# Kernel tuning notes

Measured on AMD Instinct MI355X. Metric: run time of the kernel, lower is better.

The kernel has to match this reference:

```python
import jax, jax.numpy as jnp
import numpy as np

N, E, F_IN, H, C, L = 50000, 800000, 128, 128, 47, 3
BN_EPS = 1e-5


def setup_inputs() -> dict:
    key = jax.random.key(0)
    ks = jax.random.split(key, 12)
    s = 0.1
    return {
        "x": jax.random.normal(ks[0], (N, F_IN), jnp.float32),
        "edge_index": jax.random.randint(ks[1], (2, E), 0, N, jnp.int32),
        # stacked GINConv MLP params (in_channels == hidden so all layers stack)
        "W1": jax.random.normal(ks[2], (L, F_IN, H), jnp.float32) * s,
        "b1": jnp.full((L, H), 0.01, jnp.float32),
        "gamma": jnp.ones((L, H), jnp.float32),
        "beta": jnp.zeros((L, H), jnp.float32),
        "bn_mean": jnp.zeros((L, H), jnp.float32),
        "bn_var": jnp.ones((L, H), jnp.float32),
        "W2": jax.random.normal(ks[3], (L, H, H), jnp.float32) * s,
        "b2": jnp.full((L, H), 0.01, jnp.float32),
        # head
        "lw1": jax.random.normal(ks[4], (H, H), jnp.float32) * s,
        "lb1": jnp.zeros((H,), jnp.float32),
        "lw2": jax.random.normal(ks[5], (H, C), jnp.float32) * s,
        "lb2": jnp.zeros((C,), jnp.float32),
    }


def reference(x, edge_index, W1, b1, gamma, beta, bn_mean, bn_var, W2, b2, lw1, lb1, lw2, lb2):
    src, dst = edge_index[0], edge_index[1]
    h = x
    for i in range(L):
        # GINConv: nn((1 + eps) * x + sum_{j in N(i)} x_j), eps = 0
        agg = jax.ops.segment_sum(h[src], dst, num_segments=N)  # [N, H] scatter-sum
        z = agg + h
        z = z @ W1[i] + b1[i]
        # BatchNorm1d in eval mode (running stats)
        z = (z - bn_mean[i]) * jax.lax.rsqrt(bn_var[i] + BN_EPS) * gamma[i] + beta[i]
        z = jax.nn.relu(z)
        h = jax.nn.relu(z @ W2[i] + b2[i])
    h = jax.nn.relu(h @ lw1 + lb1)
    # dropout disabled (eval mode)
    logits = h @ lw2 + lb2
    return jax.nn.log_softmax(logits, axis=-1)
```

## Files before the change

### kernel.cpp

```cpp
#include <hip/hip_runtime.h>
#include <math.h>

#define NN 50000
#define EE 800000
#define HH 128
#define LL 3
#define CC 47
#define CAP 64
#define FILL_B 2048
#define NT_TILES 782

typedef _Float16 half8 __attribute__((ext_vector_type(8)));
typedef float    f32x4 __attribute__((ext_vector_type(4)));
typedef float    f32x2 __attribute__((ext_vector_type(2)));
typedef unsigned int   u32x2 __attribute__((ext_vector_type(2)));
typedef unsigned short us8 __attribute__((ext_vector_type(8)));

__device__ __forceinline__ f32x4 mfma16(half8 a, half8 b, f32x4 c) {
    return __builtin_amdgcn_mfma_f32_16x16x32_f16(a, b, c, 0, 0, 0);
}

__device__ __forceinline__ void acc8_from_fp8(u32x2 w, float* a) {
    f32x2 p0 = __builtin_amdgcn_cvt_pk_f32_fp8(w[0], false);
    f32x2 p1 = __builtin_amdgcn_cvt_pk_f32_fp8(w[0], true);
    f32x2 p2 = __builtin_amdgcn_cvt_pk_f32_fp8(w[1], false);
    f32x2 p3 = __builtin_amdgcn_cvt_pk_f32_fp8(w[1], true);
    a[0] += p0[0]; a[1] += p0[1]; a[2] += p1[0]; a[3] += p1[1];
    a[4] += p2[0]; a[5] += p2[1]; a[6] += p3[0]; a[7] += p3[1];
}
__device__ __forceinline__ u32x2 pack8_fp8(const float* z) {
    unsigned int lo = __builtin_amdgcn_cvt_pk_fp8_f32(z[0], z[1], 0, false);
    lo = (unsigned int)__builtin_amdgcn_cvt_pk_fp8_f32(z[2], z[3], (int)lo, true);
    unsigned int hi = __builtin_amdgcn_cvt_pk_fp8_f32(z[4], z[5], 0, false);
    hi = (unsigned int)__builtin_amdgcn_cvt_pk_fp8_f32(z[6], z[7], (int)hi, true);
    u32x2 w; w[0] = lo; w[1] = hi;
    return w;
}

__global__ void k_fill_prep(const int* __restrict__ ei, int* __restrict__ cursor,
                            unsigned short* __restrict__ csr,
                            const float* __restrict__ x, const float* __restrict__ W1,
                            const float* __restrict__ W2, const float* __restrict__ lw1,
                            const float* __restrict__ lw2, const float* __restrict__ b1,
                            const float* __restrict__ gamma, const float* __restrict__ beta,
                            const float* __restrict__ bnm, const float* __restrict__ bnv,
                            unsigned char* __restrict__ x8, unsigned char* __restrict__ h8a,
                            unsigned char* __restrict__ h8b, _Float16* __restrict__ Wt1h,
                            _Float16* __restrict__ Wt2h, _Float16* __restrict__ lw1t,
                            _Float16* __restrict__ lw2t, float* __restrict__ A1f,
                            float* __restrict__ B1f) {
    if (blockIdx.x < FILL_B) {
        const int part = blockIdx.x & 7;
        const int chunk = blockIdx.x >> 3;
        const int nchunks = FILL_B >> 3;
        const int lo = part * (NN / 8);
        const int hi = (part == 7) ? NN : lo + (NN / 8);
        for (int e = chunk * 256 + threadIdx.x; e < EE; e += nchunks * 256) {
            const int d = ei[EE + e];
            if (d >= lo && d < hi) {
                const int pos = atomicAdd(&cursor[d], 1);
                if (pos < CAP) csr[(d << 6) + pos] = (unsigned short)ei[e];
            }
        }
        return;
    }
    const int i = (blockIdx.x - FILL_B) * 256 + threadIdx.x;
    const int Q0 = (NN * HH) / 8;
    const int Q1 = Q0 + LL * HH * HH;
    const int Q2 = Q1 + LL * HH * HH;
    const int Q3 = Q2 + HH * HH;
    const int Q4 = Q3 + 48 * HH;
    const int Q5 = Q4 + LL * HH;
    const int Q6 = Q5 + 3 * HH;
    if (i < Q0) {
        const f32x4* xp = (const f32x4*)x + (size_t)i * 2;
        f32x4 u = xp[0], v = xp[1];
        float z[8] = {u[0], u[1], u[2], u[3], v[0], v[1], v[2], v[3]};
        ((u32x2*)x8)[i] = pack8_fp8(z);
    } else if (i < Q1) {
        int j = i - Q0;
        int l = j / (HH * HH);
        int n = (j / HH) % HH;
        int k = j % HH;
        Wt1h[l * HH * HH + n * HH + k] = (_Float16)W1[l * HH * HH + k * HH + n];
    } else if (i < Q2) {
        int j = i - Q1;
        int l = j / (HH * HH);
        int n = (j / HH) % HH;
        int k = j % HH;
        Wt2h[l * HH * HH + n * HH + k] = (_Float16)W2[l * HH * HH + k * HH + n];
    } else if (i < Q3) {
        int j = i - Q2;
        int n = j / HH, k = j % HH;
        lw1t[n * HH + k] = (_Float16)lw1[k * HH + n];
    } else if (i < Q4) {
        int j = i - Q3;
        int n = j / HH, k = j % HH;
        lw2t[n * HH + k] = (_Float16)((n < CC) ? lw2[k * CC + n] : 0.f);
    } else if (i < Q5) {
        int j = i - Q4;
        float s = gamma[j] * rsqrtf(bnv[j] + 1e-5f);
        A1f[j] = s;
        B1f[j] = (b1[j] - bnm[j]) * s + beta[j];
    } else if (i < Q6) {
        int j = i - Q5;
        int b = j >> 7, k = j & 127;
        unsigned char* t = (b == 0) ? x8 : ((b == 1) ? h8a : h8b);
        t[(size_t)NN * HH + k] = 0;
    }
}

__device__ __forceinline__ void gather_tile8(
    const unsigned char* __restrict__ hin8, const int* __restrict__ degs,
    const unsigned short* __restrict__ csr, _Float16* Ab, int tile0, int tid, int fo) {
#pragma unroll
    for (int pass = 0; pass < 4; ++pass) {
        const int r = pass * 16 + (tid >> 4);
        const int g = tile0 + r;
        const int gg = (g < NN) ? g : NN;
        float a[8] = {0.f, 0.f, 0.f, 0.f, 0.f, 0.f, 0.f, 0.f};
        u32x2 hv = *(const u32x2*)(hin8 + (size_t)gg * HH + fo);
        acc8_from_fp8(hv, a);
        int d = (g < NN) ? degs[g] : 0;
        d = (d < CAP) ? d : CAP;
        const unsigned short* crow = csr + (gg << 6);
        for (int kk = 0; kk < d; kk += 8) {
            us8 sv = *(const us8*)(crow + kk);
            int s[8];
#pragma unroll
            for (int j = 0; j < 8; ++j) s[j] = (kk + j < d) ? (int)sv[j] : NN;
            u32x2 v[8];
#pragma unroll
            for (int j = 0; j < 8; ++j) v[j] = *(const u32x2*)(hin8 + (size_t)s[j] * HH + fo);
#pragma unroll
            for (int j = 0; j < 8; ++j) acc8_from_fp8(v[j], a);
        }
        half8 o;
#pragma unroll
        for (int j = 0; j < 8; ++j) o[j] = (_Float16)a[j];
        *(half8*)(Ab + r * 136 + fo) = o;
    }
}

__global__ __launch_bounds__(256, 4) void k_layer(
    const unsigned char* __restrict__ hin8, unsigned char* __restrict__ hout8,
    const _Float16* __restrict__ Wt1, const _Float16* __restrict__ Wt2,
    const float* __restrict__ A1, const float* __restrict__ B1,
    const float* __restrict__ b2, const int* __restrict__ degs,
    const unsigned short* __restrict__ csr) {
    __shared__ _Float16 Ab[64 * 136];
    const int tid = threadIdx.x;
    const int wave = tid >> 6, lane = tid & 63;
    const int q = lane >> 4, l15 = lane & 15;
    const int tile0 = blockIdx.x * 64;
    const int fo = (tid & 15) * 8;

    half8 Bf[2][4];
#pragma unroll
    for (int t = 0; t < 2; ++t)
#pragma unroll
        for (int kt = 0; kt < 4; ++kt)
            Bf[t][kt] = *(const half8*)(Wt1 + (wave * 32 + t * 16 + l15) * 128 + kt * 32 + q * 8);

    gather_tile8(hin8, degs, csr, Ab, tile0, tid, fo);
    __syncthreads();

    f32x4 acc[4][2];
#pragma unroll
    for (int s = 0; s < 4; ++s)
#pragma unroll
        for (int t = 0; t < 2; ++t) acc[s][t] = (f32x4){0.f, 0.f, 0.f, 0.f};
#pragma unroll
    for (int kt = 0; kt < 4; ++kt) {
        const int ko = kt * 32 + q * 8;
        half8 a0 = *(const half8*)(Ab + (0 * 16 + l15) * 136 + ko);
        half8 a1 = *(const half8*)(Ab + (1 * 16 + l15) * 136 + ko);
        half8 a2 = *(const half8*)(Ab + (2 * 16 + l15) * 136 + ko);
        half8 a3 = *(const half8*)(Ab + (3 * 16 + l15) * 136 + ko);
        acc[0][0] = mfma16(a0, Bf[0][kt], acc[0][0]);
        acc[1][0] = mfma16(a1, Bf[0][kt], acc[1][0]);
        acc[2][0] = mfma16(a2, Bf[0][kt], acc[2][0]);
        acc[3][0] = mfma16(a3, Bf[0][kt], acc[3][0]);
        acc[0][1] = mfma16(a0, Bf[1][kt], acc[0][1]);
        acc[1][1] = mfma16(a1, Bf[1][kt], acc[1][1]);
        acc[2][1] = mfma16(a2, Bf[1][kt], acc[2][1]);
        acc[3][1] = mfma16(a3, Bf[1][kt], acc[3][1]);
    }
#pragma unroll
    for (int t = 0; t < 2; ++t)
#pragma unroll
        for (int kt = 0; kt < 4; ++kt)
            Bf[t][kt] = *(const half8*)(Wt2 + (wave * 32 + t * 16 + l15) * 128 + kt * 32 + q * 8);
    __syncthreads();

#pragma unroll
    for (int t = 0; t < 2; ++t) {
        const int col = wave * 32 + t * 16 + l15;
        const float sc = A1[col], sh = B1[col];
#pragma unroll
        for (int s = 0; s < 4; ++s)
#pragma unroll
            for (int r = 0; r < 4; ++r) {
                const int row = s * 16 + q * 4 + r;
                float v = acc[s][t][r] * sc + sh;
                Ab[row * 136 + col] = (_Float16)fmaxf(v, 0.f);
            }
    }
    __syncthreads();

#pragma unroll
    for (int s = 0; s < 4; ++s)
#pragma unroll
        for (int t = 0; t < 2; ++t) acc[s][t] = (f32x4){0.f, 0.f, 0.f, 0.f};
#pragma unroll
    for (int kt = 0; kt < 4; ++kt) {
        const int ko = kt * 32 + q * 8;
        half8 a0 = *(const half8*)(Ab + (0 * 16 + l15) * 136 + ko);
        half8 a1 = *(const half8*)(Ab + (1 * 16 + l15) * 136 + ko);
        half8 a2 = *(const half8*)(Ab + (2 * 16 + l15) * 136 + ko);
        half8 a3 = *(const half8*)(Ab + (3 * 16 + l15) * 136 + ko);
        acc[0][0] = mfma16(a0, Bf[0][kt], acc[0][0]);
        acc[1][0] = mfma16(a1, Bf[0][kt], acc[1][0]);
        acc[2][0] = mfma16(a2, Bf[0][kt], acc[2][0]);
        acc[3][0] = mfma16(a3, Bf[0][kt], acc[3][0]);
        acc[0][1] = mfma16(a0, Bf[1][kt], acc[0][1]);
        acc[1][1] = mfma16(a1, Bf[1][kt], acc[1][1]);
        acc[2][1] = mfma16(a2, Bf[1][kt], acc[2][1]);
        acc[3][1] = mfma16(a3, Bf[1][kt], acc[3][1]);
    }
    __syncthreads();

#pragma unroll
    for (int t = 0; t < 2; ++t) {
        const int col = wave * 32 + t * 16 + l15;
        const float bb = b2[col];
#pragma unroll
        for (int s = 0; s < 4; ++s)
#pragma unroll
            for (int r = 0; r < 4; ++r) {
                const int row = s * 16 + q * 4 + r;
                Ab[row * 136 + col] = (_Float16)fmaxf(acc[s][t][r] + bb, 0.f);
            }
    }
    __syncthreads();

#pragma unroll
    for (int pass = 0; pass < 4; ++pass) {
        const int r = pass * 16 + (tid >> 4);
        const int g = tile0 + r;
        if (g < NN) {
            half8 z = *(const half8*)(Ab + r * 136 + fo);
            float zf[8];
#pragma unroll
            for (int j = 0; j < 8; ++j) zf[j] = (float)z[j];
            *(u32x2*)(hout8 + (size_t)g * HH + fo) = pack8_fp8(zf);
        }
    }
}

__global__ __launch_bounds__(256, 4) void k_layer_head(
    const unsigned char* __restrict__ hin8,
    const _Float16* __restrict__ Wt1, const _Float16* __restrict__ Wt2,
    const float* __restrict__ A1, const float* __restrict__ B1,
    const float* __restrict__ b2,
    const _Float16* __restrict__ lw1t, const _Float16* __restrict__ lw2t,
    const float* __restrict__ lb1, const float* __restrict__ lb2,
    float* __restrict__ out, const int* __restrict__ degs,
    const unsigned short* __restrict__ csr) {
    __shared__ _Float16 Ab[64 * 136];
    const int tid = threadIdx.x;
    const int wave = tid >> 6, lane = tid & 63;
    const int q = lane >> 4, l15 = lane & 15;
    const int tile0 = blockIdx.x * 64;
    const int fo = (tid & 15) * 8;

    half8 Bf[2][4];
#pragma unroll
    for (int t = 0; t < 2; ++t)
#pragma unroll
        for (int kt = 0; kt < 4; ++kt)
            Bf[t][kt] = *(const half8*)(Wt1 + (wave * 32 + t * 16 + l15) * 128 + kt * 32 + q * 8);

    gather_tile8(hin8, degs, csr, Ab, tile0, tid, fo);
    __syncthreads();

    f32x4 acc[4][2];
#pragma unroll
    for (int s = 0; s < 4; ++s)
#pragma unroll
        for (int t = 0; t < 2; ++t) acc[s][t] = (f32x4){0.f, 0.f, 0.f, 0.f};
#pragma unroll
    for (int kt = 0; kt < 4; ++kt) {
        const int ko = kt * 32 + q * 8;
        half8 a0 = *(const half8*)(Ab + (0 * 16 + l15) * 136 + ko);
        half8 a1 = *(const half8*)(Ab + (1 * 16 + l15) * 136 + ko);
        half8 a2 = *(const half8*)(Ab + (2 * 16 + l15) * 136 + ko);
        half8 a3 = *(const half8*)(Ab + (3 * 16 + l15) * 136 + ko);
        acc[0][0] = mfma16(a0, Bf[0][kt], acc[0][0]);
        acc[1][0] = mfma16(a1, Bf[0][kt], acc[1][0]);
        acc[2][0] = mfma16(a2, Bf[0][kt], acc[2][0]);
        acc[3][0] = mfma16(a3, Bf[0][kt], acc[3][0]);
        acc[0][1] = mfma16(a0, Bf[1][kt], acc[0][1]);
        acc[1][1] = mfma16(a1, Bf[1][kt], acc[1][1]);
        acc[2][1] = mfma16(a2, Bf[1][kt], acc[2][1]);
        acc[3][1] = mfma16(a3, Bf[1][kt], acc[3][1]);
    }
#pragma unroll
    for (int t = 0; t < 2; ++t)
#pragma unroll
        for (int kt = 0; kt < 4; ++kt)
            Bf[t][kt] = *(const half8*)(Wt2 + (wave * 32 + t * 16 + l15) * 128 + kt * 32 + q * 8);
    __syncthreads();
#pragma unroll
    for (int t = 0; t < 2; ++t) {
        const int col = wave * 32 + t * 16 + l15;
        const float sc = A1[col], sh = B1[col];
#pragma unroll
        for (int s = 0; s < 4; ++s)
#pragma unroll
            for (int r = 0; r < 4; ++r) {
                const int row = s * 16 + q * 4 + r;
                float v = acc[s][t][r] * sc + sh;
                Ab[row * 136 + col] = (_Float16)fmaxf(v, 0.f);
            }
    }
    __syncthreads();

#pragma unroll
    for (int s = 0; s < 4; ++s)
#pragma unroll
        for (int t = 0; t < 2; ++t) acc[s][t] = (f32x4){0.f, 0.f, 0.f, 0.f};
#pragma unroll
    for (int kt = 0; kt < 4; ++kt) {
        const int ko = kt * 32 + q * 8;
        half8 a0 = *(const half8*)(Ab + (0 * 16 + l15) * 136 + ko);
        half8 a1 = *(const half8*)(Ab + (1 * 16 + l15) * 136 + ko);
        half8 a2 = *(const half8*)(Ab + (2 * 16 + l15) * 136 + ko);
        half8 a3 = *(const half8*)(Ab + (3 * 16 + l15) * 136 + ko);
        acc[0][0] = mfma16(a0, Bf[0][kt], acc[0][0]);
        acc[1][0] = mfma16(a1, Bf[0][kt], acc[1][0]);
        acc[2][0] = mfma16(a2, Bf[0][kt], acc[2][0]);
        acc[3][0] = mfma16(a3, Bf[0][kt], acc[3][0]);
        acc[0][1] = mfma16(a0, Bf[1][kt], acc[0][1]);
        acc[1][1] = mfma16(a1, Bf[1][kt], acc[1][1]);
        acc[2][1] = mfma16(a2, Bf[1][kt], acc[2][1]);
        acc[3][1] = mfma16(a3, Bf[1][kt], acc[3][1]);
    }
#pragma unroll
    for (int t = 0; t < 2; ++t)
#pragma unroll
        for (int kt = 0; kt < 4; ++kt)
            Bf[t][kt] = *(const half8*)(lw1t + (wave * 32 + t * 16 + l15) * 128 + kt * 32 + q * 8);
    __syncthreads();
#pragma unroll
    for (int t = 0; t < 2; ++t) {
        const int col = wave * 32 + t * 16 + l15;
        const float bb = b2[col];
#pragma unroll
        for (int s = 0; s < 4; ++s)
#pragma unroll
            for (int r = 0; r < 4; ++r) {
                const int row = s * 16 + q * 4 + r;
                Ab[row * 136 + col] = (_Float16)fmaxf(acc[s][t][r] + bb, 0.f);
            }
    }
    __syncthreads();

#pragma unroll
    for (int s = 0; s < 4; ++s)
#pragma unroll
        for (int t = 0; t < 2; ++t) acc[s][t] = (f32x4){0.f, 0.f, 0.f, 0.f};
#pragma unroll
    for (int kt = 0; kt < 4; ++kt) {
        const int ko = kt * 32 + q * 8;
        half8 a0 = *(const half8*)(Ab + (0 * 16 + l15) * 136 + ko);
        half8 a1 = *(const half8*)(Ab + (1 * 16 + l15) * 136 + ko);
        half8 a2 = *(const half8*)(Ab + (2 * 16 + l15) * 136 + ko);
        half8 a3 = *(const half8*)(Ab + (3 * 16 + l15) * 136 + ko);
        acc[0][0] = mfma16(a0, Bf[0][kt], acc[0][0]);
        acc[1][0] = mfma16(a1, Bf[0][kt], acc[1][0]);
        acc[2][0] = mfma16(a2, Bf[0][kt], acc[2][0]);
        acc[3][0] = mfma16(a3, Bf[0][kt], acc[3][0]);
        acc[0][1] = mfma16(a0, Bf[1][kt], acc[0][1]);
        acc[1][1] = mfma16(a1, Bf[1][kt], acc[1][1]);
        acc[2][1] = mfma16(a2, Bf[1][kt], acc[2][1]);
        acc[3][1] = mfma16(a3, Bf[1][kt], acc[3][1]);
    }
    half8 Bh[4];
    if (wave < 3) {
#pragma unroll
        for (int kt = 0; kt < 4; ++kt)
            Bh[kt] = *(const half8*)(lw2t + (wave * 16 + l15) * 128 + kt * 32 + q * 8);
    }
    __syncthreads();
#pragma unroll
    for (int t = 0; t < 2; ++t) {
        const int col = wave * 32 + t * 16 + l15;
        const float bb = lb1[col];
#pragma unroll
        for (int s = 0; s < 4; ++s)
#pragma unroll
            for (int r = 0; r < 4; ++r) {
                const int row = s * 16 + q * 4 + r;
                Ab[row * 136 + col] = (_Float16)fmaxf(acc[s][t][r] + bb, 0.f);
            }
    }
    __syncthreads();

    f32x4 acc2[4];
#pragma unroll
    for (int s = 0; s < 4; ++s) acc2[s] = (f32x4){0.f, 0.f, 0.f, 0.f};
    if (wave < 3) {
#pragma unroll
        for (int kt = 0; kt < 4; ++kt) {
            const int ko = kt * 32 + q * 8;
            half8 a0 = *(const half8*)(Ab + (0 * 16 + l15) * 136 + ko);
            half8 a1 = *(const half8*)(Ab + (1 * 16 + l15) * 136 + ko);
            half8 a2 = *(const half8*)(Ab + (2 * 16 + l15) * 136 + ko);
            half8 a3 = *(const half8*)(Ab + (3 * 16 + l15) * 136 + ko);
            acc2[0] = mfma16(a0, Bh[kt], acc2[0]);
            acc2[1] = mfma16(a1, Bh[kt], acc2[1]);
            acc2[2] = mfma16(a2, Bh[kt], acc2[2]);
            acc2[3] = mfma16(a3, Bh[kt], acc2[3]);
        }
    }
    __syncthreads();

    float* Lb = (float*)Ab;
    if (wave < 3) {
        const int col = wave * 16 + l15;
        const float bb = (col < CC) ? lb2[col] : 0.f;
#pragma unroll
        for (int s = 0; s < 4; ++s)
#pragma unroll
            for (int r = 0; r < 4; ++r) {
                const int row = s * 16 + q * 4 + r;
                Lb[row * 49 + col] = acc2[s][r] + bb;
            }
    }
    __syncthreads();

    if (tid < 64) {
        const int g = tile0 + tid;
        if (g < NN) {
            float mx = -1e30f;
            for (int c = 0; c < CC; ++c) mx = fmaxf(mx, Lb[tid * 49 + c]);
            float ssum = 0.f;
            for (int c = 0; c < CC; ++c) ssum += expf(Lb[tid * 49 + c] - mx);
            const float ls = logf(ssum) + mx;
            for (int c = 0; c < CC; ++c) out[(size_t)g * CC + c] = Lb[tid * 49 + c] - ls;
        }
    }
}

extern "C" void kernel_launch(void* const* d_in, const int* in_sizes, int n_in,
                              void* d_out, int out_size, void* d_ws, size_t ws_size,
                              hipStream_t stream) {
    const float* x     = (const float*)d_in[0];
    const int*   ei    = (const int*)d_in[1];
    const float* W1    = (const float*)d_in[2];
    const float* b1    = (const float*)d_in[3];
    const float* gamma = (const float*)d_in[4];
    const float* beta  = (const float*)d_in[5];
    const float* bnm   = (const float*)d_in[6];
    const float* bnv   = (const float*)d_in[7];
    const float* W2    = (const float*)d_in[8];
    const float* b2    = (const float*)d_in[9];
    const float* lw1   = (const float*)d_in[10];
    const float* lb1   = (const float*)d_in[11];
    const float* lw2   = (const float*)d_in[12];
    const float* lb2   = (const float*)d_in[13];
    float* out = (float*)d_out;

    char* p = (char*)d_ws;
    auto carve = [&](size_t bytes) -> char* {
        char* r = p;
        p += (bytes + 255) & ~(size_t)255;
        return r;
    };
    int* cursor = (int*)carve((size_t)NN * 4);
    unsigned short* csr = (unsigned short*)carve((size_t)NN * CAP * 2);
    _Float16* Wt1h = (_Float16*)carve((size_t)LL * HH * HH * 2);
    _Float16* Wt2h = (_Float16*)carve((size_t)LL * HH * HH * 2);
    _Float16* lw1t = (_Float16*)carve((size_t)HH * HH * 2);
    _Float16* lw2t = (_Float16*)carve((size_t)48 * HH * 2);
    float* A1f = (float*)carve((size_t)LL * HH * 4);
    float* B1f = (float*)carve((size_t)LL * HH * 4);
    unsigned char* x8  = (unsigned char*)carve((size_t)(NN + 1) * HH);
    unsigned char* h8a = (unsigned char*)carve((size_t)(NN + 1) * HH);
    unsigned char* h8b = (unsigned char*)carve((size_t)(NN + 1) * HH);

    hipMemsetAsync(cursor, 0, (size_t)NN * 4, stream);
    const int prep_total = (NN * HH) / 8 + 2 * LL * HH * HH + HH * HH + 48 * HH + LL * HH + 3 * HH;
    const int prep_blocks = (prep_total + 255) / 256;
    k_fill_prep<<<FILL_B + prep_blocks, 256, 0, stream>>>(
        ei, cursor, csr, x, W1, W2, lw1, lw2, b1, gamma, beta, bnm, bnv,
        x8, h8a, h8b, Wt1h, Wt2h, lw1t, lw2t, A1f, B1f);

    k_layer<<<NT_TILES, 256, 0, stream>>>(x8, h8a, Wt1h, Wt2h, A1f, B1f, b2,
                                          cursor, csr);
    k_layer<<<NT_TILES, 256, 0, stream>>>(h8a, h8b, Wt1h + HH * HH, Wt2h + HH * HH,
                                          A1f + HH, B1f + HH, b2 + HH,
                                          cursor, csr);
    k_layer_head<<<NT_TILES, 256, 0, stream>>>(h8b, Wt1h + 2 * HH * HH, Wt2h + 2 * HH * HH,
                                               A1f + 2 * HH, B1f + 2 * HH, b2 + 2 * HH,
                                               lw1t, lw2t, lb1, lb2, out,
                                               cursor, csr);
}
```

Before: 231.3 us.

## Fuse three layer kernels into one persistent kernel with grid barriers

Merges the two GIN layer kernels and the head kernel into a single launch of 782 blocks that synchronise through an atomic grid barrier in workspace memory. This removes two kernel launch gaps and their tail effects. The gather loop is also restructured to process two rows per thread at once, giving more independent loads in flight. It relies on all 782 blocks being co-resident (4 blocks per CU of 256 threads), otherwise the barrier deadlocks, and it adds spin-wait cost at each barrier.

After: 462.6 us. 2x slower.

```diff
diff --git a/kernel.cpp b/kernel.cpp
--- a/kernel.cpp
+++ b/kernel.cpp
@@ -35,6 +35,18 @@
     hi = (unsigned int)__builtin_amdgcn_cvt_pk_fp8_f32(z[6], z[7], (int)hi, true);
     u32x2 w; w[0] = lo; w[1] = hi;
     return w;
+}
+
+__device__ __forceinline__ void grid_barrier(int* bar, int idx) {
+    __syncthreads();
+    if (threadIdx.x == 0) {
+        __threadfence();
+        __hip_atomic_fetch_add(&bar[idx], 1, __ATOMIC_RELAXED, __HIP_MEMORY_SCOPE_AGENT);
+        while (__hip_atomic_load(&bar[idx], __ATOMIC_RELAXED, __HIP_MEMORY_SCOPE_AGENT) < NT_TILES)
+            __builtin_amdgcn_s_sleep(8);
+        __threadfence();
+    }
+    __syncthreads();
 }
 
 __global__ void k_fill_prep(const int* __restrict__ ei, int* __restrict__ cursor,
@@ -114,41 +126,56 @@
     const unsigned char* __restrict__ hin8, const int* __restrict__ degs,
     const unsigned short* __restrict__ csr, _Float16* Ab, int tile0, int tid, int fo) {
 #pragma unroll
-    for (int pass = 0; pass < 4; ++pass) {
-        const int r = pass * 16 + (tid >> 4);
-        const int g = tile0 + r;
-        const int gg = (g < NN) ? g : NN;
-        float a[8] = {0.f, 0.f, 0.f, 0.f, 0.f, 0.f, 0.f, 0.f};
-        u32x2 hv = *(const u32x2*)(hin8 + (size_t)gg * HH + fo);
-        acc8_from_fp8(hv, a);
-        int d = (g < NN) ? degs[g] : 0;
-        d = (d < CAP) ? d : CAP;
-        const unsigned short* crow = csr + (gg << 6);
-        for (int kk = 0; kk < d; kk += 8) {
-            us8 sv = *(const us8*)(crow + kk);
-            int s[8];
-#pragma unroll
-            for (int j = 0; j < 8; ++j) s[j] = (kk + j < d) ? (int)sv[j] : NN;
-            u32x2 v[8];
-#pragma unroll
-            for (int j = 0; j < 8; ++j) v[j] = *(const u32x2*)(hin8 + (size_t)s[j] * HH + fo);
-#pragma unroll
-            for (int j = 0; j < 8; ++j) acc8_from_fp8(v[j], a);
+    for (int pp = 0; pp < 2; ++pp) {
+        const int rA = pp * 32 + (tid >> 4);
+        const int rB = rA + 16;
+        const int gA = tile0 + rA, gB = tile0 + rB;
+        const int ggA = (gA < NN) ? gA : NN;
+        const int ggB = (gB < NN) ? gB : NN;
+        float aA[8] = {0.f, 0.f, 0.f, 0.f, 0.f, 0.f, 0.f, 0.f};
+        float aB[8] = {0.f, 0.f, 0.f, 0.f, 0.f, 0.f, 0.f, 0.f};
+        u32x2 hvA = *(const u32x2*)(hin8 + (size_t)ggA * HH + fo);
+        u32x2 hvB = *(const u32x2*)(hin8 + (size_t)ggB * HH + fo);
+        acc8_from_fp8(hvA, aA);
+        acc8_from_fp8(hvB, aB);
+        int dA = (gA < NN) ? degs[gA] : 0; dA = (dA < CAP) ? dA : CAP;
+        int dB = (gB < NN) ? degs[gB] : 0; dB = (dB < CAP) ? dB : CAP;
+        const unsigned short* cA = csr + (ggA << 6);
+        const unsigned short* cB = csr + (ggB << 6);
+        const int dmax = (dA > dB) ? dA : dB;
+        for (int kk = 0; kk < dmax; kk += 8) {
+            us8 svA = *(const us8*)(cA + kk);
+            us8 svB = *(const us8*)(cB + kk);
+            int sA[8], sB[8];
+#pragma unroll
+            for (int j = 0; j < 8; ++j) {
+                sA[j] = (kk + j < dA) ? (int)svA[j] : NN;
+                sB[j] = (kk + j < dB) ? (int)svB[j] : NN;
+            }
+            u32x2 vA[8], vB[8];
+#pragma unroll
+            for (int j = 0; j < 8; ++j) vA[j] = *(const u32x2*)(hin8 + (size_t)sA[j] * HH + fo);
+#pragma unroll
+            for (int j = 0; j < 8; ++j) vB[j] = *(const u32x2*)(hin8 + (size_t)sB[j] * HH + fo);
+#pragma unroll
+            for (int j = 0; j < 8; ++j) acc8_from_fp8(vA[j], aA);
+#pragma unroll
+            for (int j = 0; j < 8; ++j) acc8_from_fp8(vB[j], aB);
         }
-        half8 o;
-#pragma unroll
-        for (int j = 0; j < 8; ++j) o[j] = (_Float16)a[j];
-        *(half8*)(Ab + r * 136 + fo) = o;
-    }
-}
-
-__global__ __launch_bounds__(256, 4) void k_layer(
+        half8 oA, oB;
+#pragma unroll
+        for (int j = 0; j < 8; ++j) { oA[j] = (_Float16)aA[j]; oB[j] = (_Float16)aB[j]; }
+        *(half8*)(Ab + rA * 136 + fo) = oA;
+        *(half8*)(Ab + rB * 136 + fo) = oB;
+    }
+}
+
+__device__ __forceinline__ void layer_phase(
     const unsigned char* __restrict__ hin8, unsigned char* __restrict__ hout8,
     const _Float16* __restrict__ Wt1, const _Float16* __restrict__ Wt2,
     const float* __restrict__ A1, const float* __restrict__ B1,
     const float* __restrict__ b2, const int* __restrict__ degs,
-    const unsigned short* __restrict__ csr) {
-    __shared__ _Float16 Ab[64 * 136];
+    const unsigned short* __restrict__ csr, _Float16* Ab) {
     const int tid = threadIdx.x;
     const int wave = tid >> 6, lane = tid & 63;
     const int q = lane >> 4, l15 = lane & 15;
@@ -258,7 +285,7 @@
     }
 }
 
-__global__ __launch_bounds__(256, 4) void k_layer_head(
+__device__ __forceinline__ void head_phase(
     const unsigned char* __restrict__ hin8,
     const _Float16* __restrict__ Wt1, const _Float16* __restrict__ Wt2,
     const float* __restrict__ A1, const float* __restrict__ B1,
@@ -266,8 +293,7 @@
     const _Float16* __restrict__ lw1t, const _Float16* __restrict__ lw2t,
     const float* __restrict__ lb1, const float* __restrict__ lb2,
     float* __restrict__ out, const int* __restrict__ degs,
-    const unsigned short* __restrict__ csr) {
-    __shared__ _Float16 Ab[64 * 136];
+    const unsigned short* __restrict__ csr, _Float16* Ab) {
     const int tid = threadIdx.x;
     const int wave = tid >> 6, lane = tid & 63;
     const int q = lane >> 4, l15 = lane & 15;
@@ -451,6 +477,30 @@
             for (int c = 0; c < CC; ++c) out[(size_t)g * CC + c] = Lb[tid * 49 + c] - ls;
         }
     }
+}
+
+__global__ __launch_bounds__(256, 4) void k_layers(
+    const unsigned char* __restrict__ x8, unsigned char* __restrict__ h8a,
+    unsigned char* __restrict__ h8b,
+    const _Float16* __restrict__ Wt1h, const _Float16* __restrict__ Wt2h,
+    const _Float16* __restrict__ lw1t, const _Float16* __restrict__ lw2t,
+    const float* __restrict__ A1f, const float* __restrict__ B1f,
+    const float* __restrict__ b2, const float* __restrict__ lb1,
+    const float* __restrict__ lb2, float* __restrict__ out,
+    const int* __restrict__ degs, const unsigned short* __restrict__ csr,
+    int* bar) {
+    __shared__ _Float16 Ab[64 * 136];
+
+    layer_phase(x8, h8a, Wt1h, Wt2h, A1f, B1f, b2, degs, csr, Ab);
+    grid_barrier(bar, 0);
+
+    layer_phase(h8a, h8b, Wt1h + HH * HH, Wt2h + HH * HH,
+                A1f + HH, B1f + HH, b2 + HH, degs, csr, Ab);
+    grid_barrier(bar, 1);
+
+    head_phase(h8b, Wt1h + 2 * HH * HH, Wt2h + 2 * HH * HH,
+               A1f + 2 * HH, B1f + 2 * HH, b2 + 2 * HH,
+               lw1t, lw2t, lb1, lb2, out, degs, csr, Ab);
 }
 
 extern "C" void kernel_launch(void* const* d_in, const int* in_sizes, int n_in,
@@ -479,7 +529,8 @@
         return r;
     };
     int* cursor = (int*)carve((size_t)NN * 4);
-    unsigned short* csr = (unsigned short*)carve((size_t)NN * CAP * 2);
+    int* bar = (int*)carve(256);
+    unsigned short* csr = (unsigned short*)carve((size_t)(NN + 1) * CAP * 2);
     _Float16* Wt1h = (_Float16*)carve((size_t)LL * HH * HH * 2);
     _Float16* Wt2h = (_Float16*)carve((size_t)LL * HH * HH * 2);
     _Float16* lw1t = (_Float16*)carve((size_t)HH * HH * 2);
@@ -490,20 +541,14 @@
     unsigned char* h8a = (unsigned char*)carve((size_t)(NN + 1) * HH);
     unsigned char* h8b = (unsigned char*)carve((size_t)(NN + 1) * HH);
 
-    hipMemsetAsync(cursor, 0, (size_t)NN * 4, stream);
+    hipMemsetAsync(cursor, 0, (((size_t)NN * 4 + 255) & ~(size_t)255) + 256, stream);
     const int prep_total = (NN * HH) / 8 + 2 * LL * HH * HH + HH * HH + 48 * HH + LL * HH + 3 * HH;
     const int prep_blocks = (prep_total + 255) / 256;
     k_fill_prep<<<FILL_B + prep_blocks, 256, 0, stream>>>(
         ei, cursor, csr, x, W1, W2, lw1, lw2, b1, gamma, beta, bnm, bnv,
         x8, h8a, h8b, Wt1h, Wt2h, lw1t, lw2t, A1f, B1f);
 
-    k_layer<<<NT_TILES, 256, 0, stream>>>(x8, h8a, Wt1h, Wt2h, A1f, B1f, b2,
-                                          cursor, csr);
-    k_layer<<<NT_TILES, 256, 0, stream>>>(h8a, h8b, Wt1h + HH * HH, Wt2h + HH * HH,
-                                          A1f + HH, B1f + HH, b2 + HH,
-                                          cursor, csr);
-    k_layer_head<<<NT_TILES, 256, 0, stream>>>(h8b, Wt1h + 2 * HH * HH, Wt2h + 2 * HH * HH,
-                                               A1f + 2 * HH, B1f + 2 * HH, b2 + 2 * HH,
-                                               lw1t, lw2t, lb1, lb2, out,
-                                               cursor, csr);
-}
+    k_layers<<<NT_TILES, 256, 0, stream>>>(
+        x8, h8a, h8b, Wt1h, Wt2h, lw1t, lw2t, A1f, B1f,
+        b2, lb1, lb2, out, cursor, csr, bar);
+}
```

## Split fp8 node features into two 64-byte feature planes for gather locality

Applied to the files above, without the earlier changes.

Stores the fp8 node feature arrays as two planes of 64 bytes per node, each holding half the features, instead of one 128-byte row per node. The gather processes one plane at a time with 8 threads per node, so each neighbour read touches a 64-byte segment, and the output store writes the same planar layout. The intent is to shrink the cache footprint per pass, since each plane (about 3.2 MB) can stay resident in L2 while random neighbour rows are fetched. In exchange, the CSR index list and degree loop are walked twice per node, once per plane.

Result: slower. 237.3 us (+2.6%).

```diff
diff --git a/kernel.cpp b/kernel.cpp
--- a/kernel.cpp
+++ b/kernel.cpp
@@ -9,6 +9,7 @@
 #define CAP 64
 #define FILL_B 2048
 #define NT_TILES 782
+#define PS ((size_t)(NN + 1) * 64)
 
 typedef _Float16 half8 __attribute__((ext_vector_type(8)));
 typedef float    f32x4 __attribute__((ext_vector_type(4)));
@@ -73,10 +74,12 @@
     const int Q5 = Q4 + LL * HH;
     const int Q6 = Q5 + 3 * HH;
     if (i < Q0) {
-        const f32x4* xp = (const f32x4*)x + (size_t)i * 2;
+        const int node = i >> 4, fg = i & 15;
+        const f32x4* xp = (const f32x4*)(x + (size_t)node * HH + fg * 8);
         f32x4 u = xp[0], v = xp[1];
         float z[8] = {u[0], u[1], u[2], u[3], v[0], v[1], v[2], v[3]};
-        ((u32x2*)x8)[i] = pack8_fp8(z);
+        const int plane = fg >> 3, po = (fg & 7) * 8;
+        *(u32x2*)(x8 + (size_t)plane * PS + (size_t)node * 64 + po) = pack8_fp8(z);
     } else if (i < Q1) {
         int j = i - Q0;
         int l = j / (HH * HH);
@@ -106,40 +109,66 @@
         int j = i - Q5;
         int b = j >> 7, k = j & 127;
         unsigned char* t = (b == 0) ? x8 : ((b == 1) ? h8a : h8b);
-        t[(size_t)NN * HH + k] = 0;
+        t[(size_t)(k >> 6) * PS + (size_t)NN * 64 + (k & 63)] = 0;
     }
 }
 
 __device__ __forceinline__ void gather_tile8(
     const unsigned char* __restrict__ hin8, const int* __restrict__ degs,
-    const unsigned short* __restrict__ csr, _Float16* Ab, int tile0, int tid, int fo) {
-#pragma unroll
-    for (int pass = 0; pass < 4; ++pass) {
-        const int r = pass * 16 + (tid >> 4);
-        const int g = tile0 + r;
-        const int gg = (g < NN) ? g : NN;
-        float a[8] = {0.f, 0.f, 0.f, 0.f, 0.f, 0.f, 0.f, 0.f};
-        u32x2 hv = *(const u32x2*)(hin8 + (size_t)gg * HH + fo);
-        acc8_from_fp8(hv, a);
-        int d = (g < NN) ? degs[g] : 0;
-        d = (d < CAP) ? d : CAP;
-        const unsigned short* crow = csr + (gg << 6);
-        for (int kk = 0; kk < d; kk += 8) {
-            us8 sv = *(const us8*)(crow + kk);
-            int s[8];
-#pragma unroll
-            for (int j = 0; j < 8; ++j) s[j] = (kk + j < d) ? (int)sv[j] : NN;
-            u32x2 v[8];
-#pragma unroll
-            for (int j = 0; j < 8; ++j) v[j] = *(const u32x2*)(hin8 + (size_t)s[j] * HH + fo);
-#pragma unroll
-            for (int j = 0; j < 8; ++j) acc8_from_fp8(v[j], a);
+    const unsigned short* __restrict__ csr, _Float16* Ab, int tile0, int tid) {
+    const int fo8 = (tid & 7) * 8;
+    const int nd = tid >> 3;
+#pragma unroll
+    for (int plane = 0; plane < 2; ++plane) {
+        const unsigned char* hp = hin8 + (size_t)plane * PS;
+#pragma unroll
+        for (int pass = 0; pass < 2; ++pass) {
+            const int r = pass * 32 + nd;
+            const int g = tile0 + r;
+            const int gg = (g < NN) ? g : NN;
+            float a[8] = {0.f, 0.f, 0.f, 0.f, 0.f, 0.f, 0.f, 0.f};
+            u32x2 hv = *(const u32x2*)(hp + (size_t)gg * 64 + fo8);
+            acc8_from_fp8(hv, a);
+            int d = (g < NN) ? degs[g] : 0;
+            d = (d < CAP) ? d : CAP;
+            const unsigned short* crow = csr + (gg << 6);
+            for (int kk = 0; kk < d; kk += 8) {
+                us8 sv = *(const us8*)(crow + kk);
+                int s[8];
+#pragma unroll
+                for (int j = 0; j < 8; ++j) s[j] = (kk + j < d) ? (int)sv[j] : NN;
+                u32x2 v[8];
+#pragma unroll
+                for (int j = 0; j < 8; ++j) v[j] = *(const u32x2*)(hp + (size_t)s[j] * 64 + fo8);
+#pragma unroll
+                for (int j = 0; j < 8; ++j) acc8_from_fp8(v[j], a);
+            }
+            half8 o;
+#pragma unroll
+            for (int j = 0; j < 8; ++j) o[j] = (_Float16)a[j];
+            *(half8*)(Ab + r * 136 + plane * 64 + fo8) = o;
         }
-        half8 o;
-#pragma unroll
-        for (int j = 0; j < 8; ++j) o[j] = (_Float16)a[j];
-        *(half8*)(Ab + r * 136 + fo) = o;
-    }
+    }
+}
+
+__device__ __forceinline__ void store_tile8(
+    unsigned char* __restrict__ hout8, const _Float16* Ab, int tile0, int tid) {
+    const int fo8 = (tid & 7) * 8;
+    const int nd = tid >> 3;
+#pragma unroll
+    for (int plane = 0; plane < 2; ++plane)
+#pragma unroll
+        for (int pass = 0; pass < 2; ++pass) {
+            const int r = pass * 32 + nd;
+            const int g = tile0 + r;
+            if (g < NN) {
+                half8 z = *(const half8*)(Ab + r * 136 + plane * 64 + fo8);
+                float zf[8];
+#pragma unroll
+                for (int j = 0; j < 8; ++j) zf[j] = (float)z[j];
+                *(u32x2*)(hout8 + (size_t)plane * PS + (size_t)g * 64 + fo8) = pack8_fp8(zf);
+            }
+        }
 }
 
 __global__ __launch_bounds__(256, 4) void k_layer(
@@ -153,7 +182,6 @@
     const int wave = tid >> 6, lane = tid & 63;
     const int q = lane >> 4, l15 = lane & 15;
     const int tile0 = blockIdx.x * 64;
-    const int fo = (tid & 15) * 8;
 
     half8 Bf[2][4];
 #pragma unroll
@@ -162,7 +190,7 @@
         for (int kt = 0; kt < 4; ++kt)
             Bf[t][kt] = *(const half8*)(Wt1 + (wave * 32 + t * 16 + l15) * 128 + kt * 32 + q * 8);
 
-    gather_tile8(hin8, degs, csr, Ab, tile0, tid, fo);
+    gather_tile8(hin8, degs, csr, Ab, tile0, tid);
     __syncthreads();
 
     f32x4 acc[4][2];
@@ -244,18 +272,7 @@
     }
     __syncthreads();
 
-#pragma unroll
-    for (int pass = 0; pass < 4; ++pass) {
-        const int r = pass * 16 + (tid >> 4);
-        const int g = tile0 + r;
-        if (g < NN) {
-            half8 z = *(const half8*)(Ab + r * 136 + fo);
-            float zf[8];
-#pragma unroll
-            for (int j = 0; j < 8; ++j) zf[j] = (float)z[j];
-            *(u32x2*)(hout8 + (size_t)g * HH + fo) = pack8_fp8(zf);
-        }
-    }
+    store_tile8(hout8, Ab, tile0, tid);
 }
 
 __global__ __launch_bounds__(256, 4) void k_layer_head(
@@ -272,7 +289,6 @@
     const int wave = tid >> 6, lane = tid & 63;
     const int q = lane >> 4, l15 = lane & 15;
     const int tile0 = blockIdx.x * 64;
-    const int fo = (tid & 15) * 8;
 
     half8 Bf[2][4];
 #pragma unroll
@@ -281,7 +297,7 @@
         for (int kt = 0; kt < 4; ++kt)
             Bf[t][kt] = *(const half8*)(Wt1 + (wave * 32 + t * 16 + l15) * 128 + kt * 32 + q * 8);
 
-    gather_tile8(hin8, degs, csr, Ab, tile0, tid, fo);
+    gather_tile8(hin8, degs, csr, Ab, tile0, tid);
     __syncthreads();
 
     f32x4 acc[4][2];
@@ -479,7 +495,7 @@
         return r;
     };
     int* cursor = (int*)carve((size_t)NN * 4);
-    unsigned short* csr = (unsigned short*)carve((size_t)NN * CAP * 2);
+    unsigned short* csr = (unsigned short*)carve((size_t)(NN + 1) * CAP * 2);
     _Float16* Wt1h = (_Float16*)carve((size_t)LL * HH * HH * 2);
     _Float16* Wt2h = (_Float16*)carve((size_t)LL * HH * HH * 2);
     _Float16* lw1t = (_Float16*)carve((size_t)HH * HH * 2);
```
